# Kernel optimization log

Measured on AMD Instinct MI355X. Metric: run time of the kernel, lower is better.

Reference implementation:

```python
import jax, jax.numpy as jnp
import numpy as np

B, P, K, HE, HF = 256, 128, 512, 1024, 512
D = K + HE + 2 * HF  # 2560, MLP input dim
HID = 64


def setup_inputs() -> dict:
    key = jax.random.key(0)
    ks = jax.random.split(key, 6)
    query = jax.random.normal(ks[0], (B, 1, HE), dtype=jnp.float32)
    keys = jax.random.normal(ks[1], (B, P, K), dtype=jnp.float32)
    frameLSTM_h = jax.random.normal(ks[2], (B, 1, 2 * HF), dtype=jnp.float32)
    mask = jax.random.randint(ks[3], (B, P), 0, 2, dtype=jnp.int32)
    mask = mask.at[:, 0].set(1)  # guarantee at least one unmasked player per row
    W1 = jax.random.normal(ks[4], (D, HID), dtype=jnp.float32) / np.float32(np.sqrt(D))
    W2 = jax.random.normal(ks[5], (HID, 1), dtype=jnp.float32) / np.float32(np.sqrt(HID))
    return dict(query=query, keys=keys, frameLSTM_h=frameLSTM_h, mask=mask, W1=W1, W2=W2)


def reference(query, keys, frameLSTM_h, mask, W1, W2):
    # Faithful to: cat([keys, query.repeat, frame.repeat]) @ W1 -> ReLU -> @ W2.
    # The pre-activation is linear, so splitting W1 by row-blocks is exactly the
    # same math without materializing the repeated/concatenated (B,P,D) tensor.
    W1k = W1[:K]            # (K, 64)
    W1q = W1[K:K + HE]      # (HE, 64)
    W1f = W1[K + HE:]       # (2*HF, 64)
    h = jax.nn.relu(
        jnp.einsum('bpk,kh->bph', keys, W1k)
        + jnp.einsum('boe,eh->boh', query, W1q)        # broadcasts over P
        + jnp.einsum('bof,fh->boh', frameLSTM_h, W1f)  # broadcasts over P
    )  # (B, P, 64)
    raw_scores = jnp.einsum('bph,ho->bp', h, W2)  # (B, P)
    raw_scores = jnp.where(mask == 0, -jnp.inf, raw_scores)
    weights = jax.nn.softmax(raw_scores, axis=1)  # (B, P)
    context = jnp.einsum('bp,bpk->bk', weights, keys)[:, None, :]  # (B, 1, K)
    embeddings = jnp.concatenate([context, frameLSTM_h], axis=2)   # (B, 1, K+2*HF)
    return embeddings, weights
```

## Files before the change

kernel.cpp:

```cpp
#include <hip/hip_runtime.h>
#include <hip/hip_bf16.h>
#include <cstdint>
#include <math.h>


typedef __bf16 bf16;
typedef __attribute__((ext_vector_type(8))) __bf16 bf16x8;
typedef __attribute__((ext_vector_type(4))) __bf16 bf16x4;
typedef __attribute__((ext_vector_type(4))) float f32x4;

#define NB 256
#define NP 128
#define NK 512
#define SKLD 520
#define SK_BYTES (NP * SKLD * 2)
#define SMEM_BYTES (SK_BYTES + 128*4 + 128*4 + 64*4 + 64*4)

__global__ __launch_bounds__(256) void prep_kernel(
    const float* __restrict__ query, const float* __restrict__ frame,
    const float* __restrict__ W1, bf16* __restrict__ w1kt,
    float* __restrict__ proj)
{
    const int blk = blockIdx.x;
    const int t = threadIdx.x;
    if (blk < 256) {
        __shared__ float part[4][64];
        const int b = blk;
        const int h = t & 63;
        const int g = t >> 6;
        const float* src = (g < 2) ? (query + (size_t)b * 1024 + g * 512)
                                   : (frame + (size_t)b * 1024 + (g - 2) * 512);
        const float* wrow = W1 + (size_t)(512 + g * 512) * 64 + h;
        float acc = 0.f;
#pragma unroll 8
        for (int dd = 0; dd < 512; dd++)
            acc += src[dd] * wrow[(size_t)dd * 64];
        part[g][h] = acc;
        __syncthreads();
        if (t < 64)
            proj[(size_t)b * 64 + t] = part[0][t] + part[1][t] + part[2][t] + part[3][t];
    } else {
        __shared__ float s[32][65];
        const int j = blk - 256;
        const int k0 = j * 32;
#pragma unroll
        for (int i = 0; i < 8; i++) {
            const int idx = t + 256 * i;
            const int k = idx >> 6, h = idx & 63;
            s[k][h] = W1[(size_t)(k0 + k) * 64 + h];
        }
        __syncthreads();
#pragma unroll
        for (int i = 0; i < 8; i++) {
            const int idx = t + 256 * i;
            const int h = idx >> 5, kk = idx & 31;
            w1kt[(size_t)h * 512 + k0 + kk] = (bf16)s[kk][h];
        }
    }
}

__global__ __launch_bounds__(256) void attn_kernel(
    const float* __restrict__ keys, const float* __restrict__ frame,
    const int* __restrict__ mask, const float* __restrict__ W2,
    const bf16* __restrict__ w1kt, const float* __restrict__ proj,
    float* __restrict__ out)
{
    extern __shared__ char smem[];
    bf16* sk       = (bf16*)smem;
    float* scores  = (float*)(smem + SK_BYTES);
    float* wts     = scores + 128;
    float* projl   = wts + 128;
    float* w2l     = projl + 64;

    const int b = blockIdx.x;
    const int t = threadIdx.x;

    if (t < 64) projl[t] = proj[(size_t)b * 64 + t];
    else if (t < 128) w2l[t - 64] = W2[t - 64];

    const float* kb = keys + (size_t)b * (NP * NK);
    {
        const int rowadd = (t >> 7);
        const int c0 = (t & 127) * 4;
#pragma unroll 4
        for (int i = 0; i < 64; i++) {
            const float4 v = *(const float4*)(kb + (size_t)i * 1024 + t * 4);
            bf16x4 bv;
            bv[0] = (bf16)v.x; bv[1] = (bf16)v.y; bv[2] = (bf16)v.z; bv[3] = (bf16)v.w;
            *(bf16x4*)(sk + (2 * i + rowadd) * SKLD + c0) = bv;
        }
    }
    __syncthreads();

    const int w = t >> 6;
    const int lane = t & 63;
    const int m = lane & 15;
    const int q = lane >> 4;
    const int pw = w * 32;

    f32x4 acc[2][4];
#pragma unroll
    for (int a = 0; a < 2; a++)
#pragma unroll
        for (int n = 0; n < 4; n++) acc[a][n] = (f32x4){0.f, 0.f, 0.f, 0.f};

    for (int kk = 0; kk < 16; kk++) {
        const int k0 = kk * 32 + q * 8;
        const bf16x8 A0 = *(const bf16x8*)(sk + (pw + m) * SKLD + k0);
        const bf16x8 A1 = *(const bf16x8*)(sk + (pw + 16 + m) * SKLD + k0);
#pragma unroll
        for (int nt = 0; nt < 4; nt++) {
            const bf16x8 Bf = *(const bf16x8*)(w1kt + (size_t)(nt * 16 + m) * 512 + k0);
            acc[0][nt] = __builtin_amdgcn_mfma_f32_16x16x32_bf16(A0, Bf, acc[0][nt], 0, 0, 0);
            acc[1][nt] = __builtin_amdgcn_mfma_f32_16x16x32_bf16(A1, Bf, acc[1][nt], 0, 0, 0);
        }
    }

#pragma unroll
    for (int mt = 0; mt < 2; mt++) {
        float p0 = 0.f, p1 = 0.f, p2 = 0.f, p3 = 0.f;
#pragma unroll
        for (int nt = 0; nt < 4; nt++) {
            const int h = nt * 16 + m;
            const float pr = projl[h];
            const float w2v = w2l[h];
            const f32x4 c = acc[mt][nt];
            p0 += fmaxf(c[0] + pr, 0.f) * w2v;
            p1 += fmaxf(c[1] + pr, 0.f) * w2v;
            p2 += fmaxf(c[2] + pr, 0.f) * w2v;
            p3 += fmaxf(c[3] + pr, 0.f) * w2v;
        }
#pragma unroll
        for (int off = 1; off < 16; off <<= 1) {
            p0 += __shfl_xor(p0, off);
            p1 += __shfl_xor(p1, off);
            p2 += __shfl_xor(p2, off);
            p3 += __shfl_xor(p3, off);
        }
        if (m == 0) {
            const int pbase = pw + mt * 16 + q * 4;
            scores[pbase + 0] = p0; scores[pbase + 1] = p1;
            scores[pbase + 2] = p2; scores[pbase + 3] = p3;
        }
    }
    __syncthreads();

    if (w == 0) {
        const int pa = lane, pb = lane + 64;
        float s0 = (mask[b * 128 + pa] == 0) ? -INFINITY : scores[pa];
        float s1 = (mask[b * 128 + pb] == 0) ? -INFINITY : scores[pb];
        float mx = fmaxf(s0, s1);
#pragma unroll
        for (int off = 32; off; off >>= 1) mx = fmaxf(mx, __shfl_xor(mx, off));
        float e0 = __expf(s0 - mx), e1 = __expf(s1 - mx);
        float sum = e0 + e1;
#pragma unroll
        for (int off = 32; off; off >>= 1) sum += __shfl_xor(sum, off);
        const float inv = 1.0f / sum;
        e0 *= inv; e1 *= inv;
        wts[pa] = e0; wts[pb] = e1;
        float* wout = out + (size_t)NB * 1536;
        wout[b * 128 + pa] = e0;
        wout[b * 128 + pb] = e1;
    }
    __syncthreads();

    {
        float a0 = 0.f, a1 = 0.f;
        const int c = 2 * t;
#pragma unroll 4
        for (int p = 0; p < 128; p++) {
            const float wv = wts[p];
            const uint32_t uv = *(const uint32_t*)(sk + p * SKLD + c);
            const float f0 = __uint_as_float(uv << 16);
            const float f1 = __uint_as_float(uv & 0xffff0000u);
            a0 += wv * f0;
            a1 += wv * f1;
        }
        out[(size_t)b * 1536 + c] = a0;
        out[(size_t)b * 1536 + c + 1] = a1;
    }
    {
        const float4 fv = *(const float4*)(frame + (size_t)b * 1024 + t * 4);
        *(float4*)(out + (size_t)b * 1536 + 512 + t * 4) = fv;
    }
}

extern "C" void kernel_launch(void* const* d_in, const int* in_sizes, int n_in,
                              void* d_out, int out_size, void* d_ws, size_t ws_size,
                              hipStream_t stream) {
    const float* query = (const float*)d_in[0];
    const float* keys  = (const float*)d_in[1];
    const float* frame = (const float*)d_in[2];
    const int*   mask  = (const int*)d_in[3];
    const float* W1    = (const float*)d_in[4];
    const float* W2    = (const float*)d_in[5];
    float* out = (float*)d_out;

    bf16*  w1kt = (bf16*)d_ws;
    float* proj = (float*)((char*)d_ws + 65536);

    hipFuncSetAttribute((const void*)attn_kernel,
                        hipFuncAttributeMaxDynamicSharedMemorySize, SMEM_BYTES);

    prep_kernel<<<272, 256, 0, stream>>>(query, frame, W1, w1kt, proj);
    attn_kernel<<<256, 256, SMEM_BYTES, stream>>>(keys, frame, mask, W2, w1kt, proj, out);
}
```

Before: 140.0 us.

## Fuse query/frame projection into attention kernel, overlapping with keys staging

The per-batch query/frame projection moves out of the prep kernel and into the attention kernel. There it is computed as a bf16-packed GEMV while the 16-row batches of keys loads are in flight, so the load latency is hidden behind the projection math. The prep kernel now only repacks W1 into a bf16 transposed block plus a packed bf16-pair block for the query/frame rows, which shrinks that launch to 48 blocks. In exchange the projection weights drop to bf16 precision, and holding 16 float4s per thread raises register pressure.

New measurement: 180.0 us. 28.6% more time.

```diff
diff --git a/kernel.cpp b/kernel.cpp
--- a/kernel.cpp
+++ b/kernel.cpp
@@ -14,35 +14,17 @@
 #define NK 512
 #define SKLD 520
 #define SK_BYTES (NP * SKLD * 2)
-#define SMEM_BYTES (SK_BYTES + 128*4 + 128*4 + 64*4 + 64*4)
-
-__global__ __launch_bounds__(256) void prep_kernel(
-    const float* __restrict__ query, const float* __restrict__ frame,
+#define SMEM_BYTES (SK_BYTES + 128*4 + 128*4 + 256*4 + 64*4)
+
+__global__ __launch_bounds__(256) void k0_repack(
     const float* __restrict__ W1, bf16* __restrict__ w1kt,
-    float* __restrict__ proj)
+    uint32_t* __restrict__ w1qfp)
 {
     const int blk = blockIdx.x;
     const int t = threadIdx.x;
-    if (blk < 256) {
-        __shared__ float part[4][64];
-        const int b = blk;
-        const int h = t & 63;
-        const int g = t >> 6;
-        const float* src = (g < 2) ? (query + (size_t)b * 1024 + g * 512)
-                                   : (frame + (size_t)b * 1024 + (g - 2) * 512);
-        const float* wrow = W1 + (size_t)(512 + g * 512) * 64 + h;
-        float acc = 0.f;
-#pragma unroll 8
-        for (int dd = 0; dd < 512; dd++)
-            acc += src[dd] * wrow[(size_t)dd * 64];
-        part[g][h] = acc;
-        __syncthreads();
-        if (t < 64)
-            proj[(size_t)b * 64 + t] = part[0][t] + part[1][t] + part[2][t] + part[3][t];
-    } else {
+    if (blk < 16) {
         __shared__ float s[32][65];
-        const int j = blk - 256;
-        const int k0 = j * 32;
+        const int k0 = blk * 32;
 #pragma unroll
         for (int i = 0; i < 8; i++) {
             const int idx = t + 256 * i;
@@ -56,40 +38,73 @@
             const int h = idx >> 5, kk = idx & 31;
             w1kt[(size_t)h * 512 + k0 + kk] = (bf16)s[kk][h];
         }
+    } else {
+        const int jj = blk - 16;
+#pragma unroll
+        for (int i = 0; i < 8; i++) {
+            const int idx = t + 256 * i;
+            const int dpl = idx >> 6, h = idx & 63;
+            const int dp = jj * 32 + dpl;
+            const float r0 = W1[(size_t)(512 + 2 * dp) * 64 + h];
+            const float r1 = W1[(size_t)(513 + 2 * dp) * 64 + h];
+            const uint32_t b0 = (uint32_t)__builtin_bit_cast(unsigned short, (bf16)r0);
+            const uint32_t b1 = (uint32_t)__builtin_bit_cast(unsigned short, (bf16)r1);
+            w1qfp[(size_t)dp * 64 + h] = (b1 << 16) | b0;
+        }
     }
 }
 
-__global__ __launch_bounds__(256) void attn_kernel(
-    const float* __restrict__ keys, const float* __restrict__ frame,
-    const int* __restrict__ mask, const float* __restrict__ W2,
-    const bf16* __restrict__ w1kt, const float* __restrict__ proj,
-    float* __restrict__ out)
+__global__ __launch_bounds__(256, 1) void attn_kernel(
+    const float* __restrict__ keys, const float* __restrict__ query,
+    const float* __restrict__ frame, const int* __restrict__ mask,
+    const float* __restrict__ W2, const bf16* __restrict__ w1kt,
+    const uint32_t* __restrict__ w1qfp, float* __restrict__ out)
 {
     extern __shared__ char smem[];
-    bf16* sk       = (bf16*)smem;
-    float* scores  = (float*)(smem + SK_BYTES);
-    float* wts     = scores + 128;
-    float* projl   = wts + 128;
-    float* w2l     = projl + 64;
+    bf16* sk      = (bf16*)smem;
+    float* scores = (float*)(smem + SK_BYTES);
+    float* wts    = scores + 128;
+    float* pp     = wts + 128;
+    float* w2l    = pp + 256;
 
     const int b = blockIdx.x;
     const int t = threadIdx.x;
 
-    if (t < 64) projl[t] = proj[(size_t)b * 64 + t];
-    else if (t < 128) w2l[t - 64] = W2[t - 64];
+    if (t < 64) w2l[t] = W2[t];
 
     const float* kb = keys + (size_t)b * (NP * NK);
-    {
-        const int rowadd = (t >> 7);
-        const int c0 = (t & 127) * 4;
-#pragma unroll 4
-        for (int i = 0; i < 64; i++) {
-            const float4 v = *(const float4*)(kb + (size_t)i * 1024 + t * 4);
+    const int rowadd = t >> 7;
+    const int c0 = (t & 127) * 4;
+    const int g = t >> 6;
+    const int h = t & 63;
+    const float2* s2 = (const float2*)((g < 2 ? query : frame)
+                                       + (size_t)b * 1024 + (g & 1) * 512);
+    const uint32_t* wp = w1qfp + (size_t)(g * 256) * 64 + h;
+
+    float acc = 0.f;
+#pragma unroll
+    for (int j = 0; j < 4; j++) {
+        float4 kv[16];
+#pragma unroll
+        for (int ii = 0; ii < 16; ii++)
+            kv[ii] = *(const float4*)(kb + (size_t)(j * 16 + ii) * 1024 + t * 4);
+#pragma unroll 16
+        for (int dd = 0; dd < 64; dd++) {
+            const int d = j * 64 + dd;
+            const uint32_t wv = wp[(size_t)d * 64];
+            const float2 sv = s2[d];
+            acc += sv.x * __uint_as_float(wv << 16);
+            acc += sv.y * __uint_as_float(wv & 0xffff0000u);
+        }
+#pragma unroll
+        for (int ii = 0; ii < 16; ii++) {
             bf16x4 bv;
-            bv[0] = (bf16)v.x; bv[1] = (bf16)v.y; bv[2] = (bf16)v.z; bv[3] = (bf16)v.w;
-            *(bf16x4*)(sk + (2 * i + rowadd) * SKLD + c0) = bv;
-        }
-    }
+            bv[0] = (bf16)kv[ii].x; bv[1] = (bf16)kv[ii].y;
+            bv[2] = (bf16)kv[ii].z; bv[3] = (bf16)kv[ii].w;
+            *(bf16x4*)(sk + (size_t)(2 * (j * 16 + ii) + rowadd) * SKLD + c0) = bv;
+        }
+    }
+    pp[g * 64 + h] = acc;
     __syncthreads();
 
     const int w = t >> 6;
@@ -98,11 +113,11 @@
     const int q = lane >> 4;
     const int pw = w * 32;
 
-    f32x4 acc[2][4];
+    f32x4 acc2[2][4];
 #pragma unroll
     for (int a = 0; a < 2; a++)
 #pragma unroll
-        for (int n = 0; n < 4; n++) acc[a][n] = (f32x4){0.f, 0.f, 0.f, 0.f};
+        for (int n = 0; n < 4; n++) acc2[a][n] = (f32x4){0.f, 0.f, 0.f, 0.f};
 
     for (int kk = 0; kk < 16; kk++) {
         const int k0 = kk * 32 + q * 8;
@@ -111,8 +126,8 @@
 #pragma unroll
         for (int nt = 0; nt < 4; nt++) {
             const bf16x8 Bf = *(const bf16x8*)(w1kt + (size_t)(nt * 16 + m) * 512 + k0);
-            acc[0][nt] = __builtin_amdgcn_mfma_f32_16x16x32_bf16(A0, Bf, acc[0][nt], 0, 0, 0);
-            acc[1][nt] = __builtin_amdgcn_mfma_f32_16x16x32_bf16(A1, Bf, acc[1][nt], 0, 0, 0);
+            acc2[0][nt] = __builtin_amdgcn_mfma_f32_16x16x32_bf16(A0, Bf, acc2[0][nt], 0, 0, 0);
+            acc2[1][nt] = __builtin_amdgcn_mfma_f32_16x16x32_bf16(A1, Bf, acc2[1][nt], 0, 0, 0);
         }
     }
 
@@ -121,14 +136,14 @@
         float p0 = 0.f, p1 = 0.f, p2 = 0.f, p3 = 0.f;
 #pragma unroll
         for (int nt = 0; nt < 4; nt++) {
-            const int h = nt * 16 + m;
-            const float pr = projl[h];
-            const float w2v = w2l[h];
-            const f32x4 c = acc[mt][nt];
-            p0 += fmaxf(c[0] + pr, 0.f) * w2v;
-            p1 += fmaxf(c[1] + pr, 0.f) * w2v;
-            p2 += fmaxf(c[2] + pr, 0.f) * w2v;
-            p3 += fmaxf(c[3] + pr, 0.f) * w2v;
+            const int hh = nt * 16 + m;
+            const float pv = pp[hh] + pp[64 + hh] + pp[128 + hh] + pp[192 + hh];
+            const float wv = w2l[hh];
+            const f32x4 c = acc2[mt][nt];
+            p0 += fmaxf(c[0] + pv, 0.f) * wv;
+            p1 += fmaxf(c[1] + pv, 0.f) * wv;
+            p2 += fmaxf(c[2] + pv, 0.f) * wv;
+            p3 += fmaxf(c[3] + pv, 0.f) * wv;
         }
 #pragma unroll
         for (int off = 1; off < 16; off <<= 1) {
@@ -168,14 +183,12 @@
     {
         float a0 = 0.f, a1 = 0.f;
         const int c = 2 * t;
-#pragma unroll 4
+#pragma unroll 8
         for (int p = 0; p < 128; p++) {
             const float wv = wts[p];
             const uint32_t uv = *(const uint32_t*)(sk + p * SKLD + c);
-            const float f0 = __uint_as_float(uv << 16);
-            const float f1 = __uint_as_float(uv & 0xffff0000u);
-            a0 += wv * f0;
-            a1 += wv * f1;
+            a0 += wv * __uint_as_float(uv << 16);
+            a1 += wv * __uint_as_float(uv & 0xffff0000u);
         }
         out[(size_t)b * 1536 + c] = a0;
         out[(size_t)b * 1536 + c + 1] = a1;
@@ -197,12 +210,13 @@
     const float* W2    = (const float*)d_in[5];
     float* out = (float*)d_out;
 
-    bf16*  w1kt = (bf16*)d_ws;
-    float* proj = (float*)((char*)d_ws + 65536);
+    bf16*     w1kt  = (bf16*)d_ws;
+    uint32_t* w1qfp = (uint32_t*)((char*)d_ws + (64 << 10));
 
     hipFuncSetAttribute((const void*)attn_kernel,
                         hipFuncAttributeMaxDynamicSharedMemorySize, SMEM_BYTES);
 
-    prep_kernel<<<272, 256, 0, stream>>>(query, frame, W1, w1kt, proj);
-    attn_kernel<<<256, 256, SMEM_BYTES, stream>>>(keys, frame, mask, W2, w1kt, proj, out);
+    k0_repack<<<48, 256, 0, stream>>>(W1, w1kt, w1qfp);
+    attn_kernel<<<256, 256, SMEM_BYTES, stream>>>(keys, query, frame, mask, W2,
+                                                  w1kt, w1qfp, out);
 }
```
